# Kernel tuning notes

Hardware: AMD Instinct MI355X
Metric: run time of the kernel (lower is better)

## Reference

```python
import jax, jax.numpy as jnp
import numpy as np

SIZE = 8192
DIM = 256
N = 32768
BETA = 0.25
DECAY = 0.99
EPS = 1e-5


def setup_inputs() -> dict:
    key = jax.random.key(0)
    kz, ke = jax.random.split(key)
    z = jax.random.normal(kz, (N, DIM), dtype=jnp.float32)
    # init = randn * 0.1, ema_embed_sum initialized as a clone of embeddings
    embeddings = jax.random.normal(ke, (SIZE, DIM), dtype=jnp.float32) * 0.1
    ema_embed_sum = embeddings
    ema_cluster_size = jnp.zeros((SIZE,), dtype=jnp.float32)
    usage_counter = jnp.zeros((SIZE,), dtype=jnp.int64)
    return {
        "z": z,
        "embeddings": embeddings,
        "ema_cluster_size": ema_cluster_size,
        "ema_embed_sum": ema_embed_sum,
        "usage_counter": usage_counter,
    }


def reference(z, embeddings, ema_cluster_size, ema_embed_sum, usage_counter):
    # Squared euclidean distances; argmin is identical to cdist argmin.
    z2 = jnp.sum(z * z, axis=-1, keepdims=True)              # [N, 1]
    e2 = jnp.sum(embeddings * embeddings, axis=-1)           # [K]
    d2 = z2 - 2.0 * jnp.matmul(z, embeddings.T) + e2         # [N, K]
    indices = jnp.argmin(d2, axis=-1)                         # [N]

    quantized = embeddings[indices]                           # [N, D] gather

    # usage_counter: vectorized equivalent of the per-index python loop
    counts_f = jax.ops.segment_sum(
        jnp.ones((z.shape[0],), dtype=jnp.float32), indices, num_segments=SIZE
    )                                                         # [K] == onehot.sum(0)
    new_usage = usage_counter + counts_f.astype(usage_counter.dtype)

    sg = jax.lax.stop_gradient
    commit_loss = BETA * jnp.mean((z - sg(quantized)) ** 2)
    codebook_loss = jnp.mean((quantized - sg(z)) ** 2)
    loss = commit_loss + codebook_loss

    # EMA update (training mode), all under no-grad semantics
    embed_sum = jax.ops.segment_sum(z, indices, num_segments=SIZE)  # onehot.T @ z
    new_cluster_size = DECAY * ema_cluster_size + (1.0 - DECAY) * counts_f
    new_embed_sum = DECAY * ema_embed_sum + (1.0 - DECAY) * embed_sum
    n = jnp.sum(new_cluster_size)
    cluster = (new_cluster_size + EPS) / (n + SIZE * EPS) * n
    new_embeddings = new_embed_sum / cluster[:, None]

    # straight-through estimator
    quantized_st = z + sg(quantized - z)
    return (indices, quantized_st, loss, new_embeddings, new_cluster_size,
            new_embed_sum, new_usage)
```

## Files before the change

### kernel.cpp

```cpp
#include <hip/hip_runtime.h>

#define NZ 32768
#define KE 8192
#define DD 256
#define NCHUNK 4
#define CH (KE / NCHUNK)
#define NSLICE (NCHUNK * 4)
#define ITERS ((CH / 128) * 8)
#define THR_GAP 0.05f
#define BIASF 128.0f

typedef __attribute__((ext_vector_type(8))) _Float16 f16x8;
typedef __attribute__((ext_vector_type(4))) float f32x4;
typedef unsigned int uint32;


__device__ __forceinline__ float wave_reduce_sum(float v) {
#pragma unroll
  for (int m = 32; m >= 1; m >>= 1) v += __shfl_xor(v, m, 64);
  return v;
}

__global__ void prep_kernel(const float* __restrict__ emb, unsigned short* __restrict__ e_dst,
                            float* __restrict__ e_sq, const float* __restrict__ z,
                            unsigned short* __restrict__ z_dst, float* __restrict__ z_sq,
                            const float* __restrict__ ema_cs, float* __restrict__ sema_out,
                            float* __restrict__ o_loss) {
  const int gb = blockIdx.x;
  if (gb < (KE / 4) + (NZ / 4)) {
    const float* src;
    unsigned short* dst;
    float* sq;
    int row;
    if (gb < KE / 4) {
      src = emb; dst = e_dst; sq = e_sq;
      row = gb * 4 + (threadIdx.x >> 6);
    } else {
      src = z; dst = z_dst; sq = z_sq;
      row = (gb - KE / 4) * 4 + (threadIdx.x >> 6);
    }
    const int lane = threadIdx.x & 63;
    const float4 v = *reinterpret_cast<const float4*>(src + (size_t)row * DD + lane * 4);
    alignas(8) _Float16 hv[4] = {(_Float16)v.x, (_Float16)v.y, (_Float16)v.z, (_Float16)v.w};
    *reinterpret_cast<uint2*>(dst + (size_t)row * DD + lane * 4) =
        *reinterpret_cast<const uint2*>(hv);
    float s = (v.x * v.x + v.y * v.y) + (v.z * v.z + v.w * v.w);
    s = wave_reduce_sum(s);
    if (lane == 0) sq[row] = s;
  } else {
    __shared__ float red[256];
    float s = 0.f;
    for (int i = threadIdx.x; i < KE; i += 256) s += ema_cs[i];
    red[threadIdx.x] = s;
    __syncthreads();
    for (int off = 128; off >= 1; off >>= 1) {
      if (threadIdx.x < off) red[threadIdx.x] += red[threadIdx.x + off];
      __syncthreads();
    }
    if (threadIdx.x == 0) {
      sema_out[0] = red[0];
      o_loss[0] = 0.f;
    }
  }
}


#define LSTR 32

#define LDSA(ki, r) (&ldsB[ki][r][0])

#define LOADB(RS, itv)                                                          \
  if ((itv) < ITERS) {                                                          \
    const int kb_ = ((itv) & 7) * 32;                                           \
    const size_t bo_ = (size_t)((itv) >> 3) * 128 * DD + kb_;                   \
    RS##b0 = *reinterpret_cast<const uint4*>(ef + boff0 + bo_);                 \
  }

#define WRITEB(buf, RS)                                                         \
  *reinterpret_cast<uint4*>(&ldsB[buf][ur][usw]) = RS##b0;

__launch_bounds__(512, 1)
__global__ void mfma_argmin_kernel(const unsigned short* __restrict__ zf,
                                   const unsigned short* __restrict__ ef,
                                   const float* __restrict__ e2,
                                   float4* __restrict__ pt) {
  __shared__ unsigned short ldsB[8][128][LSTR];
  __shared__ float ldsE2[CH];
  const int bid = blockIdx.x;
  const int c = (bid & 7) >> 1;
  const int mblk = ((bid >> 3) << 1) | (bid & 1);
  const int row0 = mblk * 128;
  const int cbase = c * CH;
  const int tid = threadIdx.x;
  const int wid = tid >> 6, lane = tid & 63;
  const int wr = wid >> 2, wc = wid & 3;
  const int lg = lane >> 4, l15 = lane & 15;

  const int ur = tid >> 2;
  const int usw = (((tid & 3) ^ ((ur >> 1) & 3)) << 3);
  const int csw = ((lg ^ ((l15 >> 1) & 3)) << 3);
  const size_t aoff0 = (size_t)(row0 + ur) * DD + (tid & 3) * 8;
  const size_t boff0 = (size_t)(cbase + ur) * DD + (tid & 3) * 8;

  uint32 k1[4][4], k2[4][4];
#pragma unroll
  for (int i = 0; i < 4; ++i)
#pragma unroll
    for (int r = 0; r < 4; ++r) { k1[i][r] = 0u; k2[i][r] = 0u; }

  f32x4 acc[4][2];
  f16x8 areg[8][4];

  uint4 q0_b0, q1_b0, q2_b0, q3_b0;

  LOADB(q0_, 0)
  LOADB(q1_, 1)
  LOADB(q2_, 2)
  LOADB(q3_, 3)
  for (int i = tid; i < CH; i += 512) ldsE2[i] = BIASF - 0.5f * e2[cbase + i];
#pragma unroll
  for (int ki = 0; ki < 8; ++ki) {
    const uint4 va0 = *reinterpret_cast<const uint4*>(zf + aoff0 + ki * 32);
    *reinterpret_cast<uint4*>(LDSA(ki, ur) + usw) = va0;
  }
  __syncthreads();
#pragma unroll
  for (int ki = 0; ki < 8; ++ki)
#pragma unroll
    for (int x = 0; x < 4; ++x)
      areg[ki][x] =
          *reinterpret_cast<const f16x8*>(LDSA(ki, wr * 64 + x * 16 + l15) + csw);
  __syncthreads();
  WRITEB(0, q0_)
  WRITEB(1, q1_)
  WRITEB(2, q2_)
  WRITEB(3, q3_)
  LOADB(q0_, 4)
  LOADB(q1_, 5)
  LOADB(q2_, 6)
  LOADB(q3_, 7)
  __syncthreads();

#define COMPUTE(buf, itv)                                                               \
  {                                                                                     \
    const int ki_ = (itv) & 7;                                                          \
    if (ki_ == 0) {                                                                     \
      const int e2o_ = (((itv) >> 3) << 7) + wc * 32 + l15;                             \
      const float e0_ = ldsE2[e2o_];                                                    \
      const float e1_ = ldsE2[e2o_ + 16];                                               \
      _Pragma("unroll") for (int i = 0; i < 4; ++i) {                                   \
        acc[i][0] = (f32x4)(e0_);                                                       \
        acc[i][1] = (f32x4)(e1_);                                                       \
      }                                                                                 \
    }                                                                                   \
    f16x8 bh[2];                                                                        \
    _Pragma("unroll") for (int x = 0; x < 2; ++x)                                       \
      bh[x] = *reinterpret_cast<const f16x8*>(&ldsB[buf][wc * 32 + x * 16 + l15][csw]); \
    _Pragma("unroll") for (int i = 0; i < 4; ++i)                                       \
        _Pragma("unroll") for (int j = 0; j < 2; ++j)                                   \
            acc[i][j] = __builtin_amdgcn_mfma_f32_16x16x32_f16(areg[ki_][i], bh[j], acc[i][j], 0, 0, 0); \
    if (ki_ == 7) {                                                                     \
      const uint32 tb_ = (uint32)(((itv) >> 3) << 2);                                   \
      _Pragma("unroll") for (int j = 0; j < 2; ++j) {                                   \
        const uint32 meta = tb_ | (uint32)j;                                            \
        _Pragma("unroll") for (int i = 0; i < 4; ++i)                                   \
            _Pragma("unroll") for (int r = 0; r < 4; ++r) {                             \
          const uint32 key = (__float_as_uint(acc[i][j][r]) & 0xFFFFFFC0u) | meta;      \
          const uint32 t = min(k1[i][r], key);                                          \
          k1[i][r] = max(k1[i][r], key);                                                \
          k2[i][r] = max(k2[i][r], t);                                                  \
        }                                                                               \
      }                                                                                 \
    }                                                                                   \
  }

  for (int it = 0; it < ITERS; it += 8) {
    WRITEB(4, q0_)
    LOADB(q0_, it + 8)
    COMPUTE(0, it)
    WRITEB(5, q1_)
    LOADB(q1_, it + 9)
    COMPUTE(1, it + 1)
    WRITEB(6, q2_)
    LOADB(q2_, it + 10)
    COMPUTE(2, it + 2)
    WRITEB(7, q3_)
    LOADB(q3_, it + 11)
    COMPUTE(3, it + 3)
    __syncthreads();
    WRITEB(0, q0_)
    LOADB(q0_, it + 12)
    COMPUTE(4, it + 4)
    WRITEB(1, q1_)
    LOADB(q1_, it + 13)
    COMPUTE(5, it + 5)
    WRITEB(2, q2_)
    LOADB(q2_, it + 14)
    COMPUTE(6, it + 6)
    WRITEB(3, q3_)
    LOADB(q3_, it + 15)
    COMPUTE(7, it + 7)
    __syncthreads();
  }

  float bv1[4][4], bv2[4][4];
  uint32 bpi[4][4];
  const uint32 cb_ = (uint32)(cbase + wc * 32 + l15);
#pragma unroll
  for (int i = 0; i < 4; ++i)
#pragma unroll
    for (int r = 0; r < 4; ++r) {
      const uint32 a1 = k1[i][r], a2 = k2[i][r];
      bv1[i][r] = 2.f * BIASF - 2.f * __uint_as_float(a1 & 0xFFFFFFC0u);
      bv2[i][r] = 2.f * BIASF - 2.f * __uint_as_float(a2 & 0xFFFFFFC0u);
      const uint32 c1 = cb_ + ((a1 & 60u) >> 2) * 128u + ((a1 & 3u) << 4);
      const uint32 c2 = cb_ + ((a2 & 60u) >> 2) * 128u + ((a2 & 3u) << 4);
      bpi[i][r] = c1 | (c2 << 16);
    }

#pragma unroll
  for (int m = 1; m <= 8; m <<= 1) {
#pragma unroll
    for (int i = 0; i < 4; ++i)
#pragma unroll
      for (int r = 0; r < 4; ++r) {
        const float ov1 = __shfl_xor(bv1[i][r], m, 64);
        const float ov2 = __shfl_xor(bv2[i][r], m, 64);
        const uint32 op = (uint32)__shfl_xor((int)bpi[i][r], m, 64);
        const uint32 ai1 = bpi[i][r] & 0xFFFFu, oi1 = op & 0xFFFFu;
        const bool ol = (ov1 < bv1[i][r]) || (ov1 == bv1[i][r] && oi1 < ai1);
        const float w1 = ol ? ov1 : bv1[i][r];
        const uint32 wi1 = ol ? oi1 : ai1;
        const float w2 = ol ? ov2 : bv2[i][r];
        const uint32 wi2 = ol ? (op >> 16) : (bpi[i][r] >> 16);
        const float l1 = ol ? bv1[i][r] : ov1;
        const uint32 li1 = ol ? ai1 : oi1;
        const bool s2 = (l1 < w2) || (l1 == w2 && li1 < wi2);
        bv1[i][r] = w1;
        bv2[i][r] = s2 ? l1 : w2;
        bpi[i][r] = wi1 | ((s2 ? li1 : wi2) << 16);
      }
  }
  if (l15 == 0) {
    const int slice = c * 4 + wc;
#pragma unroll
    for (int i = 0; i < 4; ++i)
#pragma unroll
      for (int r = 0; r < 4; ++r) {
        const int row = row0 + wr * 64 + i * 16 + lg * 4 + r;
        pt[(size_t)slice * NZ + row] =
            make_float4(bv1[i][r], bv2[i][r], __uint_as_float(bpi[i][r]), 0.f);
      }
  }
}

__global__ void combine_kernel(const float* __restrict__ z, const float* __restrict__ emb,
                               const float* __restrict__ z2, const float* __restrict__ e2,
                               const float4* __restrict__ pt, float* __restrict__ oidx_f,
                               int* __restrict__ oidx_i, float* __restrict__ oq,
                               float* __restrict__ oloss) {
  const int row = blockIdx.x * 4 + (threadIdx.x >> 6);
  const int lane = threadIdx.x & 63;
  const int wid = threadIdx.x >> 6;
  const float4 p = pt[(size_t)(lane & 15) * NZ + row];
  const float v1 = p.x, v2 = p.y;
  const uint32 pk = __float_as_uint(p.z);
  float m = v1;
#pragma unroll
  for (int s = 1; s <= 8; s <<= 1) m = fminf(m, __shfl_xor(m, s, 64));

  const float4 zv = *reinterpret_cast<const float4*>(z + (size_t)row * DD + lane * 4);
  const float z2r = z2[row];
  float bestd = 3.4e38f;
  int besti = KE;
#pragma unroll 1
  for (int cnum = 0; cnum < 32; ++cnum) {
    const int src = (lane & 48) | (cnum >> 1);
    const float vc = __shfl((cnum & 1) ? v2 : v1, src, 64);
    const uint32 pkc = (uint32)__shfl((int)pk, src, 64);
    const int idxc = (cnum & 1) ? (int)(pkc >> 16) : (int)(pkc & 0xFFFFu);
    if (vc < m + THR_GAP) {
      const float4 ev = *reinterpret_cast<const float4*>(emb + (size_t)idxc * DD + lane * 4);
      float s = (zv.x * ev.x + zv.y * ev.y) + (zv.z * ev.z + zv.w * ev.w);
      s = wave_reduce_sum(s);
      const float d = (z2r - 2.f * s) + e2[idxc];
      if (d < bestd || (d == bestd && idxc < besti)) { bestd = d; besti = idxc; }
    }
  }
  if (lane == 0) {
    oidx_f[row] = (float)besti;
    oidx_i[row] = besti;
  }
  const float4 qv = *reinterpret_cast<const float4*>(emb + (size_t)besti * DD + lane * 4);
  *reinterpret_cast<float4*>(oq + (size_t)row * DD + lane * 4) = qv;
  const float dx = zv.x - qv.x, dy = zv.y - qv.y, dz = zv.z - qv.z, dw = zv.w - qv.w;
  float s = (dx * dx + dy * dy) + (dz * dz + dw * dw);
  s = wave_reduce_sum(s);
  __shared__ float red[4];
  if (lane == 0) red[wid] = s;
  __syncthreads();
  if (threadIdx.x == 0) {
    const float t = (red[0] + red[1]) + (red[2] + red[3]);
    atomicAdd(oloss, t * (1.25f / ((float)NZ * (float)DD)));
  }
}

__global__ void perk_kernel(const float* __restrict__ z, const float* __restrict__ ema_cs,
                            const float* __restrict__ ema_es, const int* __restrict__ usage,
                            const int* __restrict__ idx, const float* __restrict__ sema,
                            float* __restrict__ o_emb, float* __restrict__ o_cs,
                            float* __restrict__ o_es, float* __restrict__ o_us) {
  const int k0 = blockIdx.x * 8;
  const int tid = threadIdx.x;
  __shared__ int cnt;
  __shared__ int cnt8[8];
  __shared__ int stot[8];
  __shared__ int rows[2048];
  float acc[8];
#pragma unroll
  for (int q = 0; q < 8; ++q) acc[q] = 0.f;
  if (tid < 8) stot[tid] = 0;
  for (int base = 0; base < NZ; base += 2048) {
    if (tid == 0) cnt = 0;
    if (tid < 8) cnt8[tid] = 0;
    __syncthreads();
#pragma unroll
    for (int t = 0; t < 2048; t += 256) {
      const int r = base + t + tid;
      const int q = idx[r] - k0;
      if ((unsigned)q < 8u) {
        rows[atomicAdd(&cnt, 1)] = (r << 3) | q;
        atomicAdd(&cnt8[q], 1);
      }
    }
    __syncthreads();
    const int cq = cnt;
    if (tid < 8) stot[tid] += cnt8[tid];
    for (int m = 0; m < cq; ++m) {
      const int rr = rows[m];
      const float v = z[(size_t)(rr >> 3) * DD + tid];
      const int q = rr & 7;
#pragma unroll
      for (int qq = 0; qq < 8; ++qq)
        if (qq == q) acc[qq] += v;
    }
    __syncthreads();
  }
  const float n = 0.99f * sema[0] + 0.01f * (float)NZ;
  const float dn = n + (float)KE * 1e-5f;
#pragma unroll
  for (int q = 0; q < 8; ++q) {
    const float ncs = 0.99f * ema_cs[k0 + q] + 0.01f * (float)stot[q];
    const float nes = 0.99f * ema_es[(size_t)(k0 + q) * DD + tid] + 0.01f * acc[q];
    o_es[(size_t)(k0 + q) * DD + tid] = nes;
    o_emb[(size_t)(k0 + q) * DD + tid] = nes / ((ncs + 1e-5f) / dn * n);
  }
  if (tid < 8) {
    o_cs[k0 + tid] = 0.99f * ema_cs[k0 + tid] + 0.01f * (float)stot[tid];
    o_us[k0 + tid] = (float)(usage[k0 + tid] + stot[tid]);
  }
}


extern "C" void kernel_launch(void* const* d_in, const int* in_sizes, int n_in,
                              void* d_out, int out_size, void* d_ws, size_t ws_size,
                              hipStream_t stream) {
  const float* z = (const float*)d_in[0];
  const float* emb = (const float*)d_in[1];
  const float* ema_cs = (const float*)d_in[2];
  const float* ema_es = (const float*)d_in[3];
  const int* usage = (const int*)d_in[4];

  float* out = (float*)d_out;
  float* o_idx = out;
  float* o_q = o_idx + NZ;
  float* o_loss = o_q + (size_t)NZ * DD;
  float* o_emb = o_loss + 1;
  float* o_cs = o_emb + (size_t)KE * DD;
  float* o_es = o_cs + KE;
  float* o_us = o_es + (size_t)KE * DD;

  char* w = (char*)d_ws;
  size_t off = 0;
  auto alloc = [&](size_t bytes) -> char* {
    char* r = w + off;
    off = (off + bytes + 255) & ~(size_t)255;
    return r;
  };
  float* ws_e2 = (float*)alloc(KE * 4);
  float* ws_z2 = (float*)alloc(NZ * 4);
  float* ws_sema = (float*)alloc(256);
  int* ws_idx = (int*)alloc(NZ * 4);
  float4* ws_pt = (float4*)alloc((size_t)NSLICE * NZ * 16);
  unsigned short* z_f16 = (unsigned short*)alloc((size_t)NZ * DD * 2);
  unsigned short* e_f16 = (unsigned short*)alloc((size_t)KE * DD * 2);
  (void)ws_size;

  prep_kernel<<<(KE / 4) + (NZ / 4) + 1, 256, 0, stream>>>(emb, e_f16, ws_e2, z, z_f16,
                                                           ws_z2, ema_cs, ws_sema, o_loss);

  mfma_argmin_kernel<<<(NZ / 128) * NCHUNK, 512, 0, stream>>>(z_f16, e_f16, ws_e2, ws_pt);
  combine_kernel<<<NZ / 4, 256, 0, stream>>>(z, emb, ws_z2, ws_e2, ws_pt, o_idx, ws_idx,
                                             o_q, o_loss);
  perk_kernel<<<KE / 8, 256, 0, stream>>>(z, ema_cs, ema_es, usage, ws_idx, ws_sema,
                                          o_emb, o_cs, o_es, o_us);
}
```

Baseline: 355.7 us.

## Stream codebook tiles via global_load_lds with a deeper 16-buffer pipeline

Replaces the register-staged global→LDS copy of codebook tiles with direct global_load_lds DMA into a 16-slot LDS ring, issuing loads two windows ahead. Synchronization now uses vmcnt waits plus raw barriers per window, with swizzle moved into the global source address. This is meant to remove VGPR staging and ds_write instructions and to deepen prefetch so the MFMA loop stalls less on memory. The cost is doubled LDS use and a hand-counted vmcnt scheme, which could hide a race if the counts are wrong.

```diff
diff --git a/kernel.cpp b/kernel.cpp
--- a/kernel.cpp
+++ b/kernel.cpp
@@ -66,25 +66,43 @@
 
 
 #define LSTR 32
+#define NWIN (ITERS / 4)
 
 #define LDSA(ki, r) (&ldsB[ki][r][0])
 
-#define LOADB(RS, itv)                                                          \
-  if ((itv) < ITERS) {                                                          \
+#define STAGEB(buf, itv)                                                        \
+  {                                                                             \
     const int kb_ = ((itv) & 7) * 32;                                           \
     const size_t bo_ = (size_t)((itv) >> 3) * 128 * DD + kb_;                   \
-    RS##b0 = *reinterpret_cast<const uint4*>(ef + boff0 + bo_);                 \
-  }
-
-#define WRITEB(buf, RS)                                                         \
-  *reinterpret_cast<uint4*>(&ldsB[buf][ur][usw]) = RS##b0;
+    __builtin_amdgcn_global_load_lds((const uint32*)(ef + bsw + bo_),           \
+                                     (uint32*)&ldsB[buf][wid * 16][0], 16, 0, 0); \
+  }
+
+#define STAGEW(SG, ws)                                                          \
+  {                                                                             \
+    const int s0_ = (ws) * 4;                                                   \
+    STAGEB((SG)*4 + 0, s0_ + 0)                                                 \
+    STAGEB((SG)*4 + 1, s0_ + 1)                                                 \
+    STAGEB((SG)*4 + 2, s0_ + 2)                                                 \
+    STAGEB((SG)*4 + 3, s0_ + 3)                                                 \
+  }
+
+#define VBAR4                                                  \
+  asm volatile("s_waitcnt vmcnt(4)" ::: "memory");             \
+  __builtin_amdgcn_s_barrier();                                \
+  __builtin_amdgcn_sched_barrier(0);
+
+#define VBAR0                                                  \
+  asm volatile("s_waitcnt vmcnt(0)" ::: "memory");             \
+  __builtin_amdgcn_s_barrier();                                \
+  __builtin_amdgcn_sched_barrier(0);
 
 __launch_bounds__(512, 1)
 __global__ void mfma_argmin_kernel(const unsigned short* __restrict__ zf,
                                    const unsigned short* __restrict__ ef,
                                    const float* __restrict__ e2,
                                    float4* __restrict__ pt) {
-  __shared__ unsigned short ldsB[8][128][LSTR];
+  __shared__ unsigned short ldsB[16][128][LSTR];
   __shared__ float ldsE2[CH];
   const int bid = blockIdx.x;
   const int c = (bid & 7) >> 1;
@@ -100,7 +118,7 @@
   const int usw = (((tid & 3) ^ ((ur >> 1) & 3)) << 3);
   const int csw = ((lg ^ ((l15 >> 1) & 3)) << 3);
   const size_t aoff0 = (size_t)(row0 + ur) * DD + (tid & 3) * 8;
-  const size_t boff0 = (size_t)(cbase + ur) * DD + (tid & 3) * 8;
+  const size_t bsw = (size_t)(cbase + ur) * DD + ((lane & 3) ^ ((lane >> 3) & 3)) * 8;
 
   uint32 k1[4][4], k2[4][4];
 #pragma unroll
@@ -111,12 +129,6 @@
   f32x4 acc[4][2];
   f16x8 areg[8][4];
 
-  uint4 q0_b0, q1_b0, q2_b0, q3_b0;
-
-  LOADB(q0_, 0)
-  LOADB(q1_, 1)
-  LOADB(q2_, 2)
-  LOADB(q3_, 3)
   for (int i = tid; i < CH; i += 512) ldsE2[i] = BIASF - 0.5f * e2[cbase + i];
 #pragma unroll
   for (int ki = 0; ki < 8; ++ki) {
@@ -131,21 +143,14 @@
       areg[ki][x] =
           *reinterpret_cast<const f16x8*>(LDSA(ki, wr * 64 + x * 16 + l15) + csw);
   __syncthreads();
-  WRITEB(0, q0_)
-  WRITEB(1, q1_)
-  WRITEB(2, q2_)
-  WRITEB(3, q3_)
-  LOADB(q0_, 4)
-  LOADB(q1_, 5)
-  LOADB(q2_, 6)
-  LOADB(q3_, 7)
-  __syncthreads();
-
-#define COMPUTE(buf, itv)                                                               \
+  STAGEW(0, 0)
+  STAGEW(1, 1)
+  VBAR4
+
+#define COMPUTE(buf, kil, tl)                                                           \
   {                                                                                     \
-    const int ki_ = (itv) & 7;                                                          \
-    if (ki_ == 0) {                                                                     \
-      const int e2o_ = (((itv) >> 3) << 7) + wc * 32 + l15;                             \
+    if ((kil) == 0) {                                                                   \
+      const int e2o_ = ((tl) << 7) + wc * 32 + l15;                                     \
       const float e0_ = ldsE2[e2o_];                                                    \
       const float e1_ = ldsE2[e2o_ + 16];                                               \
       _Pragma("unroll") for (int i = 0; i < 4; ++i) {                                   \
@@ -158,9 +163,9 @@
       bh[x] = *reinterpret_cast<const f16x8*>(&ldsB[buf][wc * 32 + x * 16 + l15][csw]); \
     _Pragma("unroll") for (int i = 0; i < 4; ++i)                                       \
         _Pragma("unroll") for (int j = 0; j < 2; ++j)                                   \
-            acc[i][j] = __builtin_amdgcn_mfma_f32_16x16x32_f16(areg[ki_][i], bh[j], acc[i][j], 0, 0, 0); \
-    if (ki_ == 7) {                                                                     \
-      const uint32 tb_ = (uint32)(((itv) >> 3) << 2);                                   \
+            acc[i][j] = __builtin_amdgcn_mfma_f32_16x16x32_f16(areg[kil][i], bh[j], acc[i][j], 0, 0, 0); \
+    if ((kil) == 7) {                                                                   \
+      const uint32 tb_ = (uint32)((tl) << 2);                                           \
       _Pragma("unroll") for (int j = 0; j < 2; ++j) {                                   \
         const uint32 meta = tb_ | (uint32)j;                                            \
         _Pragma("unroll") for (int i = 0; i < 4; ++i)                                   \
@@ -174,34 +179,34 @@
     }                                                                                   \
   }
 
-  for (int it = 0; it < ITERS; it += 8) {
-    WRITEB(4, q0_)
-    LOADB(q0_, it + 8)
-    COMPUTE(0, it)
-    WRITEB(5, q1_)
-    LOADB(q1_, it + 9)
-    COMPUTE(1, it + 1)
-    WRITEB(6, q2_)
-    LOADB(q2_, it + 10)
-    COMPUTE(2, it + 2)
-    WRITEB(7, q3_)
-    LOADB(q3_, it + 11)
-    COMPUTE(3, it + 3)
-    __syncthreads();
-    WRITEB(0, q0_)
-    LOADB(q0_, it + 12)
-    COMPUTE(4, it + 4)
-    WRITEB(1, q1_)
-    LOADB(q1_, it + 13)
-    COMPUTE(5, it + 5)
-    WRITEB(2, q2_)
-    LOADB(q2_, it + 14)
-    COMPUTE(6, it + 6)
-    WRITEB(3, q3_)
-    LOADB(q3_, it + 15)
-    COMPUTE(7, it + 7)
-    __syncthreads();
-  }
+#define WINDOW(G, SG, wv, P)                                                \
+  STAGEW(SG, (wv) + 2)                                                      \
+  {                                                                         \
+    const int tl_ = (wv) >> 1;                                              \
+    COMPUTE((G)*4 + 0, (P)*4 + 0, tl_)                                      \
+    COMPUTE((G)*4 + 1, (P)*4 + 1, tl_)                                      \
+    COMPUTE((G)*4 + 2, (P)*4 + 2, tl_)                                      \
+    COMPUTE((G)*4 + 3, (P)*4 + 3, tl_)                                      \
+  }                                                                         \
+  VBAR4
+
+  for (int W = 0; W < 28; W += 4) {
+    WINDOW(0, 2, W + 0, 0)
+    WINDOW(1, 3, W + 1, 1)
+    WINDOW(2, 0, W + 2, 0)
+    WINDOW(3, 1, W + 3, 1)
+  }
+  WINDOW(0, 2, 28, 0)
+  WINDOW(1, 3, 29, 1)
+  COMPUTE(8, 0, 15)
+  COMPUTE(9, 1, 15)
+  COMPUTE(10, 2, 15)
+  COMPUTE(11, 3, 15)
+  VBAR0
+  COMPUTE(12, 4, 15)
+  COMPUTE(13, 5, 15)
+  COMPUTE(14, 6, 15)
+  COMPUTE(15, 7, 15)
 
   float bv1[4][4], bv2[4][4];
   uint32 bpi[4][4];
```

After: 343.2 us. -3.5%, faster.
